# Optimization experiments

Hardware: AMD Instinct MI355X
Metric: run time of the kernel (lower is better)

Reference implementation:

```python
import jax, jax.numpy as jnp
import numpy as np
import math

BS, N_CTX, WIDTH, HEADS = 4, 2048, 1024, 16
INIT_SCALE = 0.02

def setup_inputs() -> dict:
    key = jax.random.key(0)
    ks = jax.random.split(key, 5)
    x = jax.random.normal(ks[0], (BS, N_CTX, WIDTH), dtype=jnp.float32)
    w_qkv = jax.random.normal(ks[1], (WIDTH, 3 * WIDTH), dtype=jnp.float32) * INIT_SCALE
    b_qkv = jnp.zeros((3 * WIDTH,), dtype=jnp.float32)
    w_proj = jax.random.normal(ks[2], (WIDTH, WIDTH), dtype=jnp.float32) * INIT_SCALE
    b_proj = jnp.zeros((WIDTH,), dtype=jnp.float32)
    return {"x": x, "w_qkv": w_qkv, "b_qkv": b_qkv, "w_proj": w_proj, "b_proj": b_proj}

def reference(x, w_qkv, b_qkv, w_proj, b_proj):
    bs, n_ctx, width = x.shape
    heads = HEADS
    qkv = x @ w_qkv + b_qkv  # [b, t, 3*width]
    attn_ch = (3 * width) // heads // 3  # head dim
    scale = 1.0 / math.sqrt(math.sqrt(attn_ch))
    qkv = qkv.reshape(bs, n_ctx, heads, 3 * attn_ch)
    q, k, v = jnp.split(qkv, 3, axis=-1)  # each [b, s, h, c]
    weight = jnp.einsum('bthc,bshc->bhts', q * scale, k * scale)
    weight = jax.nn.softmax(weight.astype(jnp.float32), axis=-1).astype(weight.dtype)
    out = jnp.einsum('bhts,bshc->bthc', weight, v).reshape(bs, n_ctx, width)
    return out @ w_proj + b_proj
```

## Files before the change

### kernel.cpp

```cpp
#include <hip/hip_runtime.h>
#include <stdint.h>

#define MM   8192
#define KK   1024
#define NQKV 3072
#define TT   2048
#define HH   16
#define DD   64

typedef __attribute__((ext_vector_type(8))) short bf16x8;
typedef __attribute__((ext_vector_type(4))) short short4v;
typedef __attribute__((ext_vector_type(4))) float f32x4;
typedef __attribute__((ext_vector_type(16))) float f32x16;
typedef __attribute__((ext_vector_type(4))) unsigned int u32x4;

#define MFMA16(a,b,c)  __builtin_amdgcn_mfma_f32_16x16x32_bf16(a,b,c,0,0,0)
#define MFMA32(a,b,c)  __builtin_amdgcn_mfma_f32_32x32x16_bf16(a,b,c,0,0,0)

static __device__ __forceinline__ short f2bf(float f) {
    uint32_t u = __float_as_uint(f);
    uint32_t r = (u + 0x7fffu + ((u >> 16) & 1u)) >> 16;
    return (short)r;
}

static __device__ __forceinline__ float fexp2(float x) {
    float r;
    asm("v_exp_f32 %0, %1" : "=v"(r) : "v"(x));
    return r;
}

static __device__ __forceinline__ uint32_t cvtpk(float a, float b) {
    uint32_t r;
    asm("v_cvt_pk_bf16_f32 %0, %1, %2" : "=v"(r) : "v"(a), "v"(b));
    return r;
}

static __device__ __forceinline__ void plswap(uint32_t& x, uint32_t& y) {
    asm("v_permlane32_swap_b32 %0, %1" : "+v"(x), "+v"(y));
}

static __device__ __forceinline__ float tsum16(const f32x16& p) {
    float a0 = p[0] + p[8],  a1 = p[1] + p[9];
    float a2 = p[2] + p[10], a3 = p[3] + p[11];
    float a4 = p[4] + p[12], a5 = p[5] + p[13];
    float a6 = p[6] + p[14], a7 = p[7] + p[15];
    float b0 = a0 + a4, b1 = a1 + a5, b2 = a2 + a6, b3 = a3 + a7;
    return (b0 + b2) + (b1 + b3);
}

static __device__ __forceinline__ int xcd_swz(int orig, int nwg) {
    int q = nwg >> 3, r = nwg & 7;
    int xcd = orig & 7, idx = orig >> 3;
    return (xcd < r) ? (xcd * (q + 1) + idx)
                     : (r * (q + 1) + (xcd - r) * q + idx);
}

__global__ __launch_bounds__(256) void convert_x(const float* __restrict__ x,
                                                 short* __restrict__ xb, int n) {
    int i = (blockIdx.x * 256 + threadIdx.x) * 4;
    if (i >= n) return;
    float4 v = *(const float4*)(x + i);
    short4v o;
    o[0] = f2bf(v.x); o[1] = f2bf(v.y); o[2] = f2bf(v.z); o[3] = f2bf(v.w);
    *(short4v*)(xb + i) = o;
}

__global__ __launch_bounds__(256) void transpose_w(const float* __restrict__ Wf,
                                                   short* __restrict__ Wt, int K, int N) {
    __shared__ float tile[32][33];
    const int n0 = blockIdx.x * 32, k0 = blockIdx.y * 32;
    const int tx = threadIdx.x & 31, ty = threadIdx.x >> 5;
#pragma unroll
    for (int i = 0; i < 4; ++i) {
        int k = ty + i * 8;
        tile[k][tx] = Wf[(size_t)(k0 + k) * N + n0 + tx];
    }
    __syncthreads();
#pragma unroll
    for (int i = 0; i < 4; ++i) {
        int n = ty + i * 8;
        Wt[(size_t)(n0 + n) * K + k0 + tx] = f2bf(tile[tx][n]);
    }
}

template <int N, int EPI>
__global__ __launch_bounds__(256) void gemm_bt(const short* __restrict__ A,
                                               const short* __restrict__ Bt,
                                               const float* __restrict__ bias,
                                               void* __restrict__ Cout,
                                               short* __restrict__ Kf,
                                               short* __restrict__ Vf, int K) {
    __shared__ short As[128 * 72];
    __shared__ short Bs[128 * 72];
    const int nwg = (N / 128) * (MM / 128);
    const int wg = xcd_swz(blockIdx.x, nwg);
    const int bx = wg % (N / 128), by = wg / (N / 128);
    const int tid = threadIdx.x, lane = tid & 63, wave = tid >> 6;
    const int l15 = lane & 15, lg = lane >> 4;
    const int wm = wave >> 1, wn = wave & 1;
    const int m0 = by * 128, n0 = bx * 128;

    f32x4 zero = {0.f, 0.f, 0.f, 0.f};
    f32x4 acc[4][4];
#pragma unroll
    for (int i = 0; i < 4; ++i)
#pragma unroll
        for (int j = 0; j < 4; ++j) acc[i][j] = zero;

    const int sr = tid >> 3, sc = (tid & 7) * 8;

    for (int kt = 0; kt < K; kt += 64) {
#pragma unroll
        for (int p = 0; p < 4; ++p) {
            int row = sr + p * 32;
            *(bf16x8*)(&As[row * 72 + sc]) = *(const bf16x8*)(A + (size_t)(m0 + row) * K + kt + sc);
            *(bf16x8*)(&Bs[row * 72 + sc]) = *(const bf16x8*)(Bt + (size_t)(n0 + row) * K + kt + sc);
        }
        __syncthreads();
#pragma unroll
        for (int ks = 0; ks < 2; ++ks) {
            bf16x8 af[4], bfr[4];
#pragma unroll
            for (int i = 0; i < 4; ++i)
                af[i] = *(const bf16x8*)(&As[(wm * 64 + i * 16 + l15) * 72 + ks * 32 + lg * 8]);
#pragma unroll
            for (int j = 0; j < 4; ++j)
                bfr[j] = *(const bf16x8*)(&Bs[(wn * 64 + j * 16 + l15) * 72 + ks * 32 + lg * 8]);
#pragma unroll
            for (int i = 0; i < 4; ++i)
#pragma unroll
                for (int j = 0; j < 4; ++j)
                    acc[i][j] = MFMA16(af[i], bfr[j], acc[i][j]);
        }
        __syncthreads();
    }

#pragma unroll
    for (int j = 0; j < 4; ++j) {
        int col = n0 + wn * 64 + j * 16 + l15;
        float bv = bias[col];
        if (EPI == 0) {
#pragma unroll
            for (int i = 0; i < 4; ++i) {
                int row = m0 + wm * 64 + i * 16 + lg * 4;
#pragma unroll
                for (int r = 0; r < 4; ++r)
                    ((float*)Cout)[(size_t)(row + r) * N + col] = acc[i][j][r] + bv;
            }
        } else {
            int h = col / 192, seg = col - h * 192;
#pragma unroll
            for (int i = 0; i < 4; ++i) {
#pragma unroll
                for (int r = 0; r < 4; ++r) {
                    int row = m0 + wm * 64 + i * 16 + lg * 4 + r;
                    short v = f2bf(acc[i][j][r] + bv);
                    if (seg < 64) {
                        ((short*)Cout)[(size_t)row * (HH * DD) + h * DD + seg] = v;
                    } else {
                        int key = row & (TT - 1), b = row >> 11;
                        size_t base = ((size_t)(b * HH + h) * 32 + (key >> 6)) * 4096;
                        if (seg < 128) {
                            int d = seg - 64;
                            Kf[base + ((key >> 5) & 1) * 2048 + (d >> 4) * 512
                               + ((key & 31) + 32 * ((d >> 3) & 1)) * 8 + (d & 7)] = v;
                        } else {
                            int d = seg - 128;
                            Vf[base + (d >> 5) * 2048 + ((key >> 4) & 3) * 512
                               + ((d & 31) + 32 * ((key >> 3) & 1)) * 8 + (key & 7)] = v;
                        }
                    }
                }
            }
        }
    }
}

static __device__ __forceinline__ void attn_tile(
    const bf16x8 (&kc0)[4], const bf16x8 (&kc1)[4],
    bf16x8 (&kn0)[4], bf16x8 (&kn1)[4],
    const bf16x8 (&qf)[4],
    const short* __restrict__ kfb, const short* __restrict__ vfb,
    int t, int lane8,
    f32x16& o0, f32x16& o1, float& ls) {

    int nxt = t + 1; nxt = (nxt < TT / 64) ? nxt : 0;
    const short* np = kfb + (size_t)nxt * 4096 + lane8;
#pragma unroll
    for (int dc = 0; dc < 4; ++dc) kn0[dc] = *(const bf16x8*)(np + dc * 512);
#pragma unroll
    for (int dc = 0; dc < 4; ++dc) kn1[dc] = *(const bf16x8*)(np + 2048 + dc * 512);

    const short* vp = vfb + (size_t)t * 4096 + lane8;
    bf16x8 vf0[4], vf1[4];
#pragma unroll
    for (int ks = 0; ks < 4; ++ks) vf0[ks] = *(const bf16x8*)(vp + ks * 512);
#pragma unroll
    for (int ks = 0; ks < 4; ++ks) vf1[ks] = *(const bf16x8*)(vp + 2048 + ks * 512);

    f32x16 s0, s1;
#pragma unroll
    for (int i = 0; i < 16; ++i) { s0[i] = 0.f; s1[i] = 0.f; }
#pragma unroll
    for (int dc = 0; dc < 4; ++dc) s0 = MFMA32(kc0[dc], qf[dc], s0);
#pragma unroll
    for (int dc = 0; dc < 4; ++dc) s1 = MFMA32(kc1[dc], qf[dc], s1);

#pragma unroll
    for (int i = 0; i < 16; ++i) s0[i] = fexp2(s0[i]);
#pragma unroll
    for (int i = 0; i < 16; ++i) s1[i] = fexp2(s1[i]);

    float rs = tsum16(s0) + tsum16(s1);
    rs += __shfl_xor(rs, 32);
    ls += rs;

    uint32_t a0 = cvtpk(s0[0], s0[1]),   a1 = cvtpk(s0[2], s0[3]);
    uint32_t b0 = cvtpk(s0[4], s0[5]),   b1 = cvtpk(s0[6], s0[7]);
    plswap(a0, b0); plswap(a1, b1);
    uint32_t c0 = cvtpk(s0[8], s0[9]),   c1 = cvtpk(s0[10], s0[11]);
    uint32_t d0 = cvtpk(s0[12], s0[13]), d1 = cvtpk(s0[14], s0[15]);
    plswap(c0, d0); plswap(c1, d1);
    uint32_t e0 = cvtpk(s1[0], s1[1]),   e1 = cvtpk(s1[2], s1[3]);
    uint32_t f0 = cvtpk(s1[4], s1[5]),   f1 = cvtpk(s1[6], s1[7]);
    plswap(e0, f0); plswap(e1, f1);
    uint32_t g0 = cvtpk(s1[8], s1[9]),   g1 = cvtpk(s1[10], s1[11]);
    uint32_t h0 = cvtpk(s1[12], s1[13]), h1 = cvtpk(s1[14], s1[15]);
    plswap(g0, h0); plswap(g1, h1);
    u32x4 w0 = {a0, a1, b0, b1};
    u32x4 w1 = {c0, c1, d0, d1};
    u32x4 w2 = {e0, e1, f0, f1};
    u32x4 w3 = {g0, g1, h0, h1};
    bf16x8 pa0 = __builtin_bit_cast(bf16x8, w0);
    bf16x8 pa1 = __builtin_bit_cast(bf16x8, w1);
    bf16x8 pa2 = __builtin_bit_cast(bf16x8, w2);
    bf16x8 pa3 = __builtin_bit_cast(bf16x8, w3);

    o0 = MFMA32(vf0[0], pa0, o0);
    o0 = MFMA32(vf0[1], pa1, o0);
    o0 = MFMA32(vf0[2], pa2, o0);
    o0 = MFMA32(vf0[3], pa3, o0);
    o1 = MFMA32(vf1[0], pa0, o1);
    o1 = MFMA32(vf1[1], pa1, o1);
    o1 = MFMA32(vf1[2], pa2, o1);
    o1 = MFMA32(vf1[3], pa3, o1);
}

__global__ __launch_bounds__(128) void attn_fwd(const short* __restrict__ Qt,
                                                const short* __restrict__ Kf,
                                                const short* __restrict__ Vf,
                                                short* __restrict__ Out) {
    const int wg = xcd_swz(blockIdx.x, (TT / 64) * 64);
    const int qb = wg & 31, bh = wg >> 5;
    const int b = bh >> 4, h = bh & 15;
    const int lane = threadIdx.x & 63, wave = threadIdx.x >> 6;
    const int l31 = lane & 31, hi = lane >> 5;
    const int q0 = qb * 64 + wave * 32;
    const int lane8 = lane * 8;

    const short* qptr = Qt + (size_t)(b * TT + q0 + l31) * (HH * DD) + h * DD + hi * 8;
    bf16x8 qf[4];
#pragma unroll
    for (int dc = 0; dc < 4; ++dc) qf[dc] = *(const bf16x8*)(qptr + dc * 16);

    const float cc = 0.18033688011112042f;
    {
        short* qs = (short*)qf;
#pragma unroll
        for (int i = 0; i < 32; ++i) {
            float v = __uint_as_float(((uint32_t)(uint16_t)qs[i]) << 16) * cc;
            qs[i] = f2bf(v);
        }
    }

    const short* kfb = Kf + (size_t)bh * 32 * 4096;
    const short* vfb = Vf + (size_t)bh * 32 * 4096;

    f32x16 o0, o1;
#pragma unroll
    for (int i = 0; i < 16; ++i) { o0[i] = 0.f; o1[i] = 0.f; }
    float ls = 0.f;

    bf16x8 kA0[4], kA1[4], kB0[4], kB1[4];
#pragma unroll
    for (int dc = 0; dc < 4; ++dc) kA0[dc] = *(const bf16x8*)(kfb + dc * 512 + lane8);
#pragma unroll
    for (int dc = 0; dc < 4; ++dc) kA1[dc] = *(const bf16x8*)(kfb + 2048 + dc * 512 + lane8);

    for (int t = 0; t < TT / 64; t += 2) {
        attn_tile(kA0, kA1, kB0, kB1, qf, kfb, vfb, t,     lane8, o0, o1, ls);
        attn_tile(kB0, kB1, kA0, kA1, qf, kfb, vfb, t + 1, lane8, o0, o1, ls);
    }

    float inv = 1.0f / ls;
    short* orow = Out + (size_t)(b * TT + q0 + l31) * (HH * DD) + h * DD;
#pragma unroll
    for (int g = 0; g < 4; ++g) {
        short4v v0, v1;
#pragma unroll
        for (int r = 0; r < 4; ++r) {
            v0[r] = f2bf(o0[g * 4 + r] * inv);
            v1[r] = f2bf(o1[g * 4 + r] * inv);
        }
        *(short4v*)(orow + g * 8 + hi * 4) = v0;
        *(short4v*)(orow + 32 + g * 8 + hi * 4) = v1;
    }
}

extern "C" void kernel_launch(void* const* d_in, const int* in_sizes, int n_in,
                              void* d_out, int out_size, void* d_ws, size_t ws_size,
                              hipStream_t stream) {
    const float* x      = (const float*)d_in[0];
    const float* w_qkv  = (const float*)d_in[1];
    const float* b_qkv  = (const float*)d_in[2];
    const float* w_proj = (const float*)d_in[3];
    const float* b_proj = (const float*)d_in[4];
    float* out = (float*)d_out;

    char* ws = (char*)d_ws;
    short* xb     = (short*)(ws);
    short* wqkvt  = (short*)(ws + 16777216);
    short* wprojt = (short*)(ws + 23068672);
    short* qt     = (short*)(ws + 25165824);
    short* kf     = (short*)(ws + 41943040);
    short* vf     = (short*)(ws + 58720256);
    short* ao     = (short*)(ws + 75497472);

    convert_x<<<8192, 256, 0, stream>>>(x, xb, MM * KK);
    transpose_w<<<dim3(NQKV / 32, KK / 32), 256, 0, stream>>>(w_qkv, wqkvt, KK, NQKV);
    transpose_w<<<dim3(KK / 32, KK / 32), 256, 0, stream>>>(w_proj, wprojt, KK, KK);
    gemm_bt<NQKV, 1><<<(NQKV / 128) * (MM / 128), 256, 0, stream>>>(
        xb, wqkvt, b_qkv, qt, kf, vf, KK);
    attn_fwd<<<(TT / 64) * 64, 128, 0, stream>>>(qt, kf, vf, ao);
    gemm_bt<KK, 0><<<(KK / 128) * (MM / 128), 256, 0, stream>>>(
        ao, wprojt, b_proj, out, nullptr, nullptr, KK);
}
```

Measured before the change: 205.2 us.

## Rewrite GEMMs as 256x256 tiles with double-buffered direct-to-LDS loads

Result: slower. 244.2 us (+19.0%).

```diff
diff --git a/kernel.cpp b/kernel.cpp
--- a/kernel.cpp
+++ b/kernel.cpp
@@ -16,6 +16,11 @@
 
 #define MFMA16(a,b,c)  __builtin_amdgcn_mfma_f32_16x16x32_bf16(a,b,c,0,0,0)
 #define MFMA32(a,b,c)  __builtin_amdgcn_mfma_f32_32x32x16_bf16(a,b,c,0,0,0)
+
+#define GLOAD_LDS16(g, l)                                                      \
+    __builtin_amdgcn_global_load_lds(                                          \
+        (const __attribute__((address_space(1))) void*)(g),                    \
+        (__attribute__((address_space(3))) void*)(l), 16, 0, 0)
 
 static __device__ __forceinline__ short f2bf(float f) {
     uint32_t u = __float_as_uint(f);
@@ -83,78 +88,108 @@
     }
 }
 
+static __device__ __forceinline__ void stage256(const short* __restrict__ A,
+                                                const short* __restrict__ Bt,
+                                                short* As, short* Bs,
+                                                int m0, int n0, int K, int kt,
+                                                int wave, int lane) {
+    const int lr = lane >> 3, lc = (lane & 7) * 8;
+#pragma unroll
+    for (int c = 0; c < 4; ++c) {
+        int row = wave * 32 + c * 8;
+        GLOAD_LDS16(A + (size_t)(m0 + row + lr) * K + kt + lc, As + row * 64);
+    }
+#pragma unroll
+    for (int c = 0; c < 4; ++c) {
+        int row = wave * 32 + c * 8;
+        GLOAD_LDS16(Bt + (size_t)(n0 + row + lr) * K + kt + lc, Bs + row * 64);
+    }
+}
+
 template <int N, int EPI>
-__global__ __launch_bounds__(256) void gemm_bt(const short* __restrict__ A,
-                                               const short* __restrict__ Bt,
-                                               const float* __restrict__ bias,
-                                               void* __restrict__ Cout,
-                                               short* __restrict__ Kf,
-                                               short* __restrict__ Vf, int K) {
-    __shared__ short As[128 * 72];
-    __shared__ short Bs[128 * 72];
-    const int nwg = (N / 128) * (MM / 128);
+__global__ __launch_bounds__(512, 2) void gemm256(const short* __restrict__ A,
+                                                  const short* __restrict__ Bt,
+                                                  const float* __restrict__ bias,
+                                                  void* __restrict__ Cout,
+                                                  short* __restrict__ Kf,
+                                                  short* __restrict__ Vf, int K) {
+    __shared__ short As[2][256 * 64];
+    __shared__ short Bs[2][256 * 64];
+    const int nwg = (N / 256) * (MM / 256);
     const int wg = xcd_swz(blockIdx.x, nwg);
-    const int bx = wg % (N / 128), by = wg / (N / 128);
+    const int bx = wg % (N / 256), by = wg / (N / 256);
+    const int m0 = by * 256, n0 = bx * 256;
     const int tid = threadIdx.x, lane = tid & 63, wave = tid >> 6;
+    const int wm = wave >> 2, wn = wave & 3;
     const int l15 = lane & 15, lg = lane >> 4;
-    const int wm = wave >> 1, wn = wave & 1;
-    const int m0 = by * 128, n0 = bx * 128;
+
+    float bv[4];
+#pragma unroll
+    for (int j = 0; j < 4; ++j) bv[j] = bias[n0 + wn * 64 + j * 16 + l15];
 
     f32x4 zero = {0.f, 0.f, 0.f, 0.f};
-    f32x4 acc[4][4];
-#pragma unroll
-    for (int i = 0; i < 4; ++i)
+    f32x4 acc[8][4];
+#pragma unroll
+    for (int i = 0; i < 8; ++i)
 #pragma unroll
         for (int j = 0; j < 4; ++j) acc[i][j] = zero;
 
-    const int sr = tid >> 3, sc = (tid & 7) * 8;
-
-    for (int kt = 0; kt < K; kt += 64) {
-#pragma unroll
-        for (int p = 0; p < 4; ++p) {
-            int row = sr + p * 32;
-            *(bf16x8*)(&As[row * 72 + sc]) = *(const bf16x8*)(A + (size_t)(m0 + row) * K + kt + sc);
-            *(bf16x8*)(&Bs[row * 72 + sc]) = *(const bf16x8*)(Bt + (size_t)(n0 + row) * K + kt + sc);
+    stage256(A, Bt, &As[0][0], &Bs[0][0], m0, n0, K, 0, wave, lane);
+    stage256(A, Bt, &As[1][0], &Bs[1][0], m0, n0, K, 64, wave, lane);
+
+    const int nt = K >> 6;
+    for (int t = 0; t < nt; ++t) {
+        if (t < nt - 1) asm volatile("s_waitcnt vmcnt(8)" ::: "memory");
+        else            asm volatile("s_waitcnt vmcnt(0)" ::: "memory");
+        __builtin_amdgcn_sched_barrier(0);
+        __builtin_amdgcn_s_barrier();
+        asm volatile("" ::: "memory");
+
+        const short* as = &As[t & 1][(wm * 128 + l15) * 64 + lg * 8];
+        const short* bs = &Bs[t & 1][(wn * 64 + l15) * 64 + lg * 8];
+#pragma unroll
+        for (int ks = 0; ks < 2; ++ks) {
+            bf16x8 a[8], b[4];
+#pragma unroll
+            for (int i = 0; i < 8; ++i) a[i] = *(const bf16x8*)(as + i * 1024 + ks * 32);
+#pragma unroll
+            for (int j = 0; j < 4; ++j) b[j] = *(const bf16x8*)(bs + j * 1024 + ks * 32);
+            __builtin_amdgcn_s_setprio(1);
+#pragma unroll
+            for (int i = 0; i < 8; ++i)
+#pragma unroll
+                for (int j = 0; j < 4; ++j)
+                    acc[i][j] = MFMA16(a[i], b[j], acc[i][j]);
+            __builtin_amdgcn_s_setprio(0);
         }
-        __syncthreads();
-#pragma unroll
-        for (int ks = 0; ks < 2; ++ks) {
-            bf16x8 af[4], bfr[4];
-#pragma unroll
-            for (int i = 0; i < 4; ++i)
-                af[i] = *(const bf16x8*)(&As[(wm * 64 + i * 16 + l15) * 72 + ks * 32 + lg * 8]);
-#pragma unroll
-            for (int j = 0; j < 4; ++j)
-                bfr[j] = *(const bf16x8*)(&Bs[(wn * 64 + j * 16 + l15) * 72 + ks * 32 + lg * 8]);
-#pragma unroll
-            for (int i = 0; i < 4; ++i)
-#pragma unroll
-                for (int j = 0; j < 4; ++j)
-                    acc[i][j] = MFMA16(af[i], bfr[j], acc[i][j]);
-        }
-        __syncthreads();
+        asm volatile("" ::: "memory");
+        __builtin_amdgcn_s_barrier();
+        asm volatile("" ::: "memory");
+        if (t + 2 < nt)
+            stage256(A, Bt, &As[t & 1][0], &Bs[t & 1][0], m0, n0, K,
+                     (t + 2) * 64, wave, lane);
     }
 
 #pragma unroll
     for (int j = 0; j < 4; ++j) {
         int col = n0 + wn * 64 + j * 16 + l15;
-        float bv = bias[col];
+        float bvj = bv[j];
         if (EPI == 0) {
 #pragma unroll
-            for (int i = 0; i < 4; ++i) {
-                int row = m0 + wm * 64 + i * 16 + lg * 4;
+            for (int i = 0; i < 8; ++i) {
+                int row = m0 + wm * 128 + i * 16 + lg * 4;
 #pragma unroll
                 for (int r = 0; r < 4; ++r)
-                    ((float*)Cout)[(size_t)(row + r) * N + col] = acc[i][j][r] + bv;
+                    ((float*)Cout)[(size_t)(row + r) * N + col] = acc[i][j][r] + bvj;
             }
         } else {
             int h = col / 192, seg = col - h * 192;
 #pragma unroll
-            for (int i = 0; i < 4; ++i) {
+            for (int i = 0; i < 8; ++i) {
 #pragma unroll
                 for (int r = 0; r < 4; ++r) {
-                    int row = m0 + wm * 64 + i * 16 + lg * 4 + r;
-                    short v = f2bf(acc[i][j][r] + bv);
+                    int row = m0 + wm * 128 + i * 16 + lg * 4 + r;
+                    short v = f2bf(acc[i][j][r] + bvj);
                     if (seg < 64) {
                         ((short*)Cout)[(size_t)row * (HH * DD) + h * DD + seg] = v;
                     } else {
@@ -329,9 +364,9 @@
     convert_x<<<8192, 256, 0, stream>>>(x, xb, MM * KK);
     transpose_w<<<dim3(NQKV / 32, KK / 32), 256, 0, stream>>>(w_qkv, wqkvt, KK, NQKV);
     transpose_w<<<dim3(KK / 32, KK / 32), 256, 0, stream>>>(w_proj, wprojt, KK, KK);
-    gemm_bt<NQKV, 1><<<(NQKV / 128) * (MM / 128), 256, 0, stream>>>(
+    gemm256<NQKV, 1><<<(NQKV / 256) * (MM / 256), 512, 0, stream>>>(
         xb, wqkvt, b_qkv, qt, kf, vf, KK);
     attn_fwd<<<(TT / 64) * 64, 128, 0, stream>>>(qt, kf, vf, ao);
-    gemm_bt<KK, 0><<<(KK / 128) * (MM / 128), 256, 0, stream>>>(
+    gemm256<KK, 0><<<(KK / 256) * (MM / 256), 512, 0, stream>>>(
         ao, wprojt, b_proj, out, nullptr, nullptr, KK);
 }
```

## Replace QKV GEMM with 256x256 8-wave ping-pong kernel using direct-to-LDS loads

Applied to the files above, without the earlier changes.

Measured after the change: 269.4 us. +31.3%, slower.

```diff
diff --git a/kernel.cpp b/kernel.cpp
--- a/kernel.cpp
+++ b/kernel.cpp
@@ -16,6 +16,11 @@
 
 #define MFMA16(a,b,c)  __builtin_amdgcn_mfma_f32_16x16x32_bf16(a,b,c,0,0,0)
 #define MFMA32(a,b,c)  __builtin_amdgcn_mfma_f32_32x32x16_bf16(a,b,c,0,0,0)
+
+#define GLOAD_LDS16(g, l)                                                      \
+    __builtin_amdgcn_global_load_lds(                                          \
+        (const __attribute__((address_space(1))) void*)(g),                    \
+        (__attribute__((address_space(3))) void*)(l), 16, 0, 0)
 
 static __device__ __forceinline__ short f2bf(float f) {
     uint32_t u = __float_as_uint(f);
@@ -83,13 +88,11 @@
     }
 }
 
-template <int N, int EPI>
+template <int N>
 __global__ __launch_bounds__(256) void gemm_bt(const short* __restrict__ A,
                                                const short* __restrict__ Bt,
                                                const float* __restrict__ bias,
-                                               void* __restrict__ Cout,
-                                               short* __restrict__ Kf,
-                                               short* __restrict__ Vf, int K) {
+                                               float* __restrict__ Cout, int K) {
     __shared__ short As[128 * 72];
     __shared__ short Bs[128 * 72];
     const int nwg = (N / 128) * (MM / 128);
@@ -134,41 +137,155 @@
         }
         __syncthreads();
     }
-
 #pragma unroll
     for (int j = 0; j < 4; ++j) {
         int col = n0 + wn * 64 + j * 16 + l15;
         float bv = bias[col];
-        if (EPI == 0) {
-#pragma unroll
-            for (int i = 0; i < 4; ++i) {
-                int row = m0 + wm * 64 + i * 16 + lg * 4;
-#pragma unroll
-                for (int r = 0; r < 4; ++r)
-                    ((float*)Cout)[(size_t)(row + r) * N + col] = acc[i][j][r] + bv;
-            }
-        } else {
-            int h = col / 192, seg = col - h * 192;
-#pragma unroll
-            for (int i = 0; i < 4; ++i) {
-#pragma unroll
-                for (int r = 0; r < 4; ++r) {
-                    int row = m0 + wm * 64 + i * 16 + lg * 4 + r;
-                    short v = f2bf(acc[i][j][r] + bv);
-                    if (seg < 64) {
-                        ((short*)Cout)[(size_t)row * (HH * DD) + h * DD + seg] = v;
+#pragma unroll
+        for (int i = 0; i < 4; ++i) {
+            int row = m0 + wm * 64 + i * 16 + lg * 4;
+#pragma unroll
+            for (int r = 0; r < 4; ++r)
+                Cout[(size_t)(row + r) * N + col] = acc[i][j][r] + bv;
+        }
+    }
+}
+
+template <int N>
+__global__ __launch_bounds__(512) void gemm8p(const short* __restrict__ A,
+                                              const short* __restrict__ Bt,
+                                              const float* __restrict__ bias,
+                                              short* __restrict__ Qt,
+                                              short* __restrict__ Kf,
+                                              short* __restrict__ Vf, int K) {
+    __shared__ short As[2][2][128 * 64];
+    __shared__ short Bs[2][2][128 * 64];
+    const int nwg = (N / 256) * (MM / 256);
+    const int wg = xcd_swz(blockIdx.x, nwg);
+    const int bx = wg % (N / 256), by = wg / (N / 256);
+    const int m0 = by * 256, n0 = bx * 256;
+    const int tid = threadIdx.x, lane = tid & 63, wave = tid >> 6;
+    const int wm = wave >> 2, wn = wave & 3;
+    const int l15 = lane & 15, lg = lane >> 4;
+    const int lr = lane >> 3, lc = (lane & 7) * 8;
+    const int arow = wave * 16;
+
+    float bv[4];
+#pragma unroll
+    for (int j = 0; j < 4; ++j) bv[j] = bias[n0 + wn * 64 + j * 16 + l15];
+
+    f32x4 zero = {0.f, 0.f, 0.f, 0.f};
+    f32x4 acc[8][4];
+#pragma unroll
+    for (int i = 0; i < 8; ++i)
+#pragma unroll
+        for (int j = 0; j < 4; ++j) acc[i][j] = zero;
+
+    auto stageA = [&](int s, int kt) {
+#pragma unroll
+        for (int h2 = 0; h2 < 2; ++h2)
+#pragma unroll
+            for (int c = 0; c < 2; ++c)
+                GLOAD_LDS16(A + (size_t)(m0 + h2 * 128 + arow + c * 8 + lr) * K + kt + lc,
+                            &As[s][h2][(arow + c * 8) * 64]);
+    };
+    auto stageB = [&](int s, int kt) {
+#pragma unroll
+        for (int h2 = 0; h2 < 2; ++h2)
+#pragma unroll
+            for (int c = 0; c < 2; ++c)
+                GLOAD_LDS16(Bt + (size_t)(n0 + h2 * 128 + arow + c * 8 + lr) * K + kt + lc,
+                            &Bs[s][h2][(arow + c * 8) * 64]);
+    };
+
+#define PHASE(SLOT, MH, NH, STG, KTS, DRAIN)                                   \
+    {                                                                          \
+        bf16x8 af[4][2], bfv[2][2];                                            \
+        _Pragma("unroll")                                                      \
+        for (int ii = 0; ii < 4; ++ii)                                         \
+            _Pragma("unroll")                                                  \
+            for (int ks = 0; ks < 2; ++ks)                                     \
+                af[ii][ks] = *(const bf16x8*)(&As[SLOT][wm][                   \
+                    ((MH) * 64 + ii * 16 + l15) * 64 + ks * 32 + lg * 8]);     \
+        _Pragma("unroll")                                                      \
+        for (int jj = 0; jj < 2; ++jj)                                         \
+            _Pragma("unroll")                                                  \
+            for (int ks = 0; ks < 2; ++ks)                                     \
+                bfv[jj][ks] = *(const bf16x8*)(&Bs[SLOT][wn >> 1][             \
+                    ((wn & 1) * 64 + (NH) * 32 + jj * 16 + l15) * 64           \
+                    + ks * 32 + lg * 8]);                                      \
+        if ((STG) == 1) stageA((SLOT) ^ 1, KTS);                               \
+        if ((STG) == 2) stageB((SLOT) ^ 1, KTS);                               \
+        if (DRAIN) {                                                           \
+            asm volatile("s_waitcnt vmcnt(0)" ::: "memory");                   \
+            __builtin_amdgcn_sched_barrier(0);                                 \
+        }                                                                      \
+        asm volatile("" ::: "memory");                                         \
+        __builtin_amdgcn_s_barrier();                                          \
+        asm volatile("" ::: "memory");                                         \
+        __builtin_amdgcn_s_setprio(1);                                         \
+        _Pragma("unroll")                                                      \
+        for (int ii = 0; ii < 4; ++ii)                                         \
+            _Pragma("unroll")                                                  \
+            for (int jj = 0; jj < 2; ++jj)                                     \
+                _Pragma("unroll")                                              \
+                for (int ks = 0; ks < 2; ++ks)                                 \
+                    acc[(MH) * 4 + ii][(NH) * 2 + jj] =                        \
+                        MFMA16(af[ii][ks], bfv[jj][ks],                        \
+                               acc[(MH) * 4 + ii][(NH) * 2 + jj]);             \
+        __builtin_amdgcn_s_setprio(0);                                         \
+        asm volatile("" ::: "memory");                                         \
+        __builtin_amdgcn_s_barrier();                                          \
+        asm volatile("" ::: "memory");                                         \
+    }
+
+    stageA(0, 0);
+    stageB(0, 0);
+    asm volatile("s_waitcnt vmcnt(0)" ::: "memory");
+    __builtin_amdgcn_sched_barrier(0);
+    __builtin_amdgcn_s_barrier();
+    asm volatile("" ::: "memory");
+
+    const int nt = K >> 6;
+    for (int u = 0; u < nt / 2; ++u) {
+        const int kt1 = (2 * u + 1) * 64;
+        const int kt2 = (2 * u + 2) * 64;
+        const int s2 = (2 * u + 2 < nt) ? 1 : 0;
+        PHASE(0, 0, 0, 1, kt1, false);
+        PHASE(0, 0, 1, 2, kt1, false);
+        PHASE(0, 1, 0, 0, 0, false);
+        PHASE(0, 1, 1, 0, 0, true);
+        PHASE(1, 0, 0, s2 * 1, kt2, false);
+        PHASE(1, 0, 1, s2 * 2, kt2, false);
+        PHASE(1, 1, 0, 0, 0, false);
+        PHASE(1, 1, 1, 0, 0, true);
+    }
+#undef PHASE
+
+#pragma unroll
+    for (int j = 0; j < 4; ++j) {
+        int col = n0 + wn * 64 + j * 16 + l15;
+        float bvj = bv[j];
+        int h = col / 192, seg = col - h * 192;
+#pragma unroll
+        for (int i = 0; i < 8; ++i) {
+#pragma unroll
+            for (int r = 0; r < 4; ++r) {
+                int row = m0 + wm * 128 + i * 16 + lg * 4 + r;
+                short v = f2bf(acc[i][j][r] + bvj);
+                if (seg < 64) {
+                    Qt[(size_t)row * (HH * DD) + h * DD + seg] = v;
+                } else {
+                    int key = row & (TT - 1), b = row >> 11;
+                    size_t base = ((size_t)(b * HH + h) * 32 + (key >> 6)) * 4096;
+                    if (seg < 128) {
+                        int d = seg - 64;
+                        Kf[base + ((key >> 5) & 1) * 2048 + (d >> 4) * 512
+                           + ((key & 31) + 32 * ((d >> 3) & 1)) * 8 + (d & 7)] = v;
                     } else {
-                        int key = row & (TT - 1), b = row >> 11;
-                        size_t base = ((size_t)(b * HH + h) * 32 + (key >> 6)) * 4096;
-                        if (seg < 128) {
-                            int d = seg - 64;
-                            Kf[base + ((key >> 5) & 1) * 2048 + (d >> 4) * 512
-                               + ((key & 31) + 32 * ((d >> 3) & 1)) * 8 + (d & 7)] = v;
-                        } else {
-                            int d = seg - 128;
-                            Vf[base + (d >> 5) * 2048 + ((key >> 4) & 3) * 512
-                               + ((d & 31) + 32 * ((key >> 3) & 1)) * 8 + (key & 7)] = v;
-                        }
+                        int d = seg - 128;
+                        Vf[base + (d >> 5) * 2048 + ((key >> 4) & 3) * 512
+                           + ((d & 31) + 32 * ((key >> 3) & 1)) * 8 + (key & 7)] = v;
                     }
                 }
             }
@@ -329,9 +446,9 @@
     convert_x<<<8192, 256, 0, stream>>>(x, xb, MM * KK);
     transpose_w<<<dim3(NQKV / 32, KK / 32), 256, 0, stream>>>(w_qkv, wqkvt, KK, NQKV);
     transpose_w<<<dim3(KK / 32, KK / 32), 256, 0, stream>>>(w_proj, wprojt, KK, KK);
-    gemm_bt<NQKV, 1><<<(NQKV / 128) * (MM / 128), 256, 0, stream>>>(
+    gemm8p<NQKV><<<(NQKV / 256) * (MM / 256), 512, 0, stream>>>(
         xb, wqkvt, b_qkv, qt, kf, vf, KK);
     attn_fwd<<<(TT / 64) * 64, 128, 0, stream>>>(qt, kf, vf, ao);
-    gemm_bt<KK, 0><<<(KK / 128) * (MM / 128), 256, 0, stream>>>(
-        ao, wprojt, b_proj, out, nullptr, nullptr, KK);
-}
+    gemm_bt<KK><<<(KK / 128) * (MM / 128), 256, 0, stream>>>(
+        ao, wprojt, b_proj, out, KK);
+}
```
